# Performance work log

Hardware: AMD Instinct MI355X
Metric: run time of the kernel (lower is better)

Reference implementation:

```python
import jax, jax.numpy as jnp
import numpy as np

B, CQ, CR, HID, H, W = 8, 1024, 512, 256, 48, 48


def setup_inputs() -> dict:
    key = jax.random.key(0)
    ks = jax.random.split(key, 6)
    return {
        "query_features": jax.random.normal(ks[0], (B, CQ, H, W), dtype=jnp.float32),
        "reference_features": jax.random.normal(ks[1], (B, CR, H, W), dtype=jnp.float32),
        "Wq": jax.random.normal(ks[2], (HID, CQ), dtype=jnp.float32) * (1.0 / np.sqrt(CQ)),
        "bq": jax.random.normal(ks[3], (HID,), dtype=jnp.float32) * 0.01,
        "Wk": jax.random.normal(ks[4], (HID, CR), dtype=jnp.float32) * (1.0 / np.sqrt(CR)),
        "bk": jax.random.normal(ks[5], (HID,), dtype=jnp.float32) * 0.01,
    }


def reference(query_features, reference_features, Wq, bq, Wk, bk):
    b, _, h1, w1 = query_features.shape
    h2, w2 = reference_features.shape[-2:]
    # 1x1 convs == per-pixel linear projections
    Q = jnp.einsum("oc,bchw->bohw", Wq, query_features) + bq[None, :, None, None]
    K = jnp.einsum("oc,bchw->bohw", Wk, reference_features) + bk[None, :, None, None]
    # V: [b, c_ref, h2*w2]
    V = reference_features.reshape(b, reference_features.shape[1], h2 * w2)
    # attention logits: [b, h1, w1, h2*w2]
    attn = jnp.einsum("bcij,bckl->bijkl", Q, K).reshape(b, h1, w1, h2 * w2)
    attn = jax.nn.softmax(attn, axis=3)
    # weighted sum of V: [b, c_ref, h1, w1]
    attended = jnp.einsum("bijp,bcp->bcij", attn, V)
    return attended
```

## Files before the change

kernel.cpp:

```cpp
#include <hip/hip_runtime.h>

#define BB   8
#define PP   2304
#define CQD  1024
#define CRD  512
#define HIDD 256
#define GB   4
#define NKB  36
#define LOG2E 1.4426950408889634f

typedef float f32x4 __attribute__((ext_vector_type(4)));
typedef __bf16 bf16x8 __attribute__((ext_vector_type(8)));
typedef unsigned short u16x8 __attribute__((ext_vector_type(8)));
typedef unsigned short u16x4 __attribute__((ext_vector_type(4)));
typedef unsigned int u32x4 __attribute__((ext_vector_type(4)));
typedef unsigned short ushort_t;

__device__ __forceinline__ unsigned short f2bf(float f) {
  unsigned int u = __float_as_uint(f);
  u += 0x7fffu + ((u >> 16) & 1u);
  return (unsigned short)(u >> 16);
}
__device__ __forceinline__ float bf2f(unsigned short h) {
  return __uint_as_float(((unsigned int)h) << 16);
}
__device__ __forceinline__ bf16x8 load_bf8(const ushort_t* p) {
  return *(const bf16x8*)p;
}
__device__ __forceinline__ void async16(const void* g, void* l) {
  __builtin_amdgcn_global_load_lds(
      (const __attribute__((address_space(1))) unsigned int*)g,
      (__attribute__((address_space(3))) unsigned int*)l, 16, 0, 0);
}

#define MFMA16(a, b, c) __builtin_amdgcn_mfma_f32_16x16x32_bf16((a), (b), (c), 0, 0, 0)

__global__ __launch_bounds__(256) void wcast_kernel(
    const float* __restrict__ W, ushort_t* __restrict__ Wh,
    ushort_t* __restrict__ Wl) {
  const size_t i = ((size_t)blockIdx.x * 256 + threadIdx.x) * 8;
  float4 a = *(const float4*)(W + i);
  float4 b2 = *(const float4*)(W + i + 4);
  float av[8] = {a.x, a.y, a.z, a.w, b2.x, b2.y, b2.z, b2.w};
  u16x8 h, l;
#pragma unroll
  for (int j = 0; j < 8; ++j) {
    unsigned short hh = f2bf(av[j]);
    h[j] = hh;
    l[j] = f2bf(av[j] - bf2f(hh));
  }
  *(u16x8*)(Wh + i) = h;
  *(u16x8*)(Wl + i) = l;
}

template <int C, bool WV>
__global__ __launch_bounds__(256) void tcast_kernel(
    const float* __restrict__ X, ushort_t* __restrict__ Th,
    ushort_t* __restrict__ Tl, ushort_t* __restrict__ Vb) {
  const int b = blockIdx.z;
  const int p0 = blockIdx.x * 64;
  const int c0 = blockIdx.y * 64;
  const int tid = threadIdx.x;

  __shared__ unsigned int HL[64][66];

  {
    const int cr = tid >> 2;
    const int ch = tid & 3;
    const float* src = X + ((size_t)b * C + c0 + cr) * PP + p0 + ch * 16;
    u16x8 vcast[2];
#pragma unroll
    for (int i = 0; i < 4; ++i) {
      float4 v = *(const float4*)(src + i * 4);
      float vv[4] = {v.x, v.y, v.z, v.w};
#pragma unroll
      for (int k = 0; k < 4; ++k) {
        unsigned short h = f2bf(vv[k]);
        unsigned short l = f2bf(vv[k] - bf2f(h));
        HL[ch * 16 + i * 4 + k][cr] =
            (unsigned int)h | ((unsigned int)l << 16);
        if (WV) vcast[i >> 1][(i & 1) * 4 + k] = h;
      }
    }
    if (WV) {
      ushort_t* vd = Vb + ((size_t)b * C + c0 + cr) * PP + p0 + ch * 16;
      *(u16x8*)(vd) = vcast[0];
      *(u16x8*)(vd + 8) = vcast[1];
    }
  }
  __syncthreads();
  {
    const int pr = tid >> 2;
    const int pc = tid & 3;
    u16x8 hv[2], lv[2];
#pragma unroll
    for (int m = 0; m < 2; ++m)
#pragma unroll
      for (int j = 0; j < 8; ++j) {
        unsigned int wb = HL[pr][pc * 16 + m * 8 + j];
        hv[m][j] = (unsigned short)(wb & 0xffffu);
        lv[m][j] = (unsigned short)(wb >> 16);
      }
    const size_t obase = ((size_t)b * PP + p0 + pr) * C + c0 + pc * 16;
    *(u16x8*)(Th + obase) = hv[0];
    *(u16x8*)(Th + obase + 8) = hv[1];
    *(u16x8*)(Tl + obase) = lv[0];
    *(u16x8*)(Tl + obase + 8) = lv[1];
  }
}

template <int C>
__global__ __launch_bounds__(256, 2) void projgemm_kernel(
    const ushort_t* __restrict__ Wh, const ushort_t* __restrict__ Wl,
    const ushort_t* __restrict__ Xh, const ushort_t* __restrict__ Xl,
    const float* __restrict__ bias, ushort_t* __restrict__ Oh,
    ushort_t* __restrict__ Ol) {
  const int bp0 = blockIdx.x * 128;
  const int o0 = blockIdx.y * 128;
  const int tid = threadIdx.x;
  const int lane = tid & 63;
  const int w = tid >> 6;
  const int l15 = lane & 15;
  const int quad = lane >> 4;
  const int wm = w & 1;
  const int wn = w >> 1;

  __shared__ __align__(16) ushort_t AB[2][4][128][32];

  f32x4 acc[4][4] = {};

  const ushort_t* srcs[4] = {Wh + (size_t)o0 * C, Wl + (size_t)o0 * C,
                             Xh + (size_t)bp0 * C, Xl + (size_t)bp0 * C};
  const ushort_t* mysrc = srcs[w];
  const int r16 = lane >> 2;
  const int c8 = (lane & 3) * 8;

  auto stage = [&](int cs, int buf) {
    const ushort_t* sp = mysrc + cs * 32 + c8;
#pragma unroll
    for (int i = 0; i < 8; ++i)
      async16(sp + (size_t)(i * 16 + r16) * C, &AB[buf][w][i * 16][0]);
  };

  stage(0, 0);
  __syncthreads();

  const int NS = C / 32;
  for (int cs = 0; cs < NS; ++cs) {
    const int buf = cs & 1;
    if (cs + 1 < NS) stage(cs + 1, buf ^ 1);

    bf16x8 ah[4], al[4], bh[4], bl[4];
#pragma unroll
    for (int mt = 0; mt < 4; ++mt) {
      const int row = wm * 64 + mt * 16 + l15;
      ah[mt] = load_bf8(&AB[buf][0][row][quad * 8]);
      al[mt] = load_bf8(&AB[buf][1][row][quad * 8]);
    }
#pragma unroll
    for (int nt = 0; nt < 4; ++nt) {
      const int row = wn * 64 + nt * 16 + l15;
      bh[nt] = load_bf8(&AB[buf][2][row][quad * 8]);
      bl[nt] = load_bf8(&AB[buf][3][row][quad * 8]);
    }
#pragma unroll
    for (int mt = 0; mt < 4; ++mt)
#pragma unroll
      for (int nt = 0; nt < 4; ++nt) {
        acc[mt][nt] = MFMA16(ah[mt], bh[nt], acc[mt][nt]);
        acc[mt][nt] = MFMA16(al[mt], bh[nt], acc[mt][nt]);
        acc[mt][nt] = MFMA16(ah[mt], bl[nt], acc[mt][nt]);
      }
    __syncthreads();
  }

#pragma unroll
  for (int mt = 0; mt < 4; ++mt) {
    const int ob = o0 + wm * 64 + mt * 16 + quad * 4;
    float bv[4];
#pragma unroll
    for (int r = 0; r < 4; ++r) bv[r] = bias[ob + r];
#pragma unroll
    for (int nt = 0; nt < 4; ++nt) {
      const int bp = bp0 + wn * 64 + nt * 16 + l15;
      u16x4 hs, ls;
#pragma unroll
      for (int r = 0; r < 4; ++r) {
        float v2 = acc[mt][nt][r] + bv[r];
        unsigned short h = f2bf(v2);
        hs[r] = h;
        ls[r] = f2bf(v2 - bf2f(h));
      }
      const size_t base = (size_t)bp * HIDD + ob;
      *(u16x4*)(Oh + base) = hs;
      *(u16x4*)(Ol + base) = ls;
    }
  }
}

template <int C>
__global__ __launch_bounds__(256) void proj_kernel(
    const float* __restrict__ X, const float* __restrict__ W,
    const float* __restrict__ bias, ushort_t* __restrict__ Oh,
    ushort_t* __restrict__ Ol) {
  const int b = blockIdx.z;
  const int p0 = blockIdx.y * 64;
  const int o0 = blockIdx.x * 64;
  const int tid = threadIdx.x;
  const int lane = tid & 63;
  const int wave = tid >> 6;
  const int wm = wave & 1;
  const int wn = wave >> 1;
  const int l15 = lane & 15;
  const int quad = lane >> 4;

  __shared__ ushort_t Xh[64][40];
  __shared__ ushort_t Xl[64][40];

  f32x4 acc[2][2] = {};
  const float* Xb = X + (size_t)b * C * PP;
  const int cc = tid >> 3;
  const int ppo = (tid & 7) * 8;

  for (int c0 = 0; c0 < C; c0 += 32) {
    const float* src = Xb + (size_t)(c0 + cc) * PP + p0 + ppo;
    float4 v0 = *(const float4*)(src);
    float4 v1 = *(const float4*)(src + 4);
    float vv[8] = {v0.x, v0.y, v0.z, v0.w, v1.x, v1.y, v1.z, v1.w};
#pragma unroll
    for (int j = 0; j < 8; ++j) {
      unsigned short h = f2bf(vv[j]);
      Xh[ppo + j][cc] = h;
      Xl[ppo + j][cc] = f2bf(vv[j] - bf2f(h));
    }
    __syncthreads();

    bf16x8 wh[2], wl[2];
#pragma unroll
    for (int mt = 0; mt < 2; ++mt) {
      const float* wsrc =
          W + (size_t)(o0 + wm * 32 + mt * 16 + l15) * C + c0 + quad * 8;
      float4 a0 = *(const float4*)(wsrc);
      float4 a1 = *(const float4*)(wsrc + 4);
      float av[8] = {a0.x, a0.y, a0.z, a0.w, a1.x, a1.y, a1.z, a1.w};
      u16x8 hh, ll;
#pragma unroll
      for (int j = 0; j < 8; ++j) {
        unsigned short h = f2bf(av[j]);
        hh[j] = h;
        ll[j] = f2bf(av[j] - bf2f(h));
      }
      wh[mt] = __builtin_bit_cast(bf16x8, hh);
      wl[mt] = __builtin_bit_cast(bf16x8, ll);
    }

#pragma unroll
    for (int nt = 0; nt < 2; ++nt) {
      const int pr = wn * 32 + nt * 16 + l15;
      bf16x8 xh = load_bf8(&Xh[pr][quad * 8]);
      bf16x8 xl = load_bf8(&Xl[pr][quad * 8]);
#pragma unroll
      for (int mt = 0; mt < 2; ++mt) {
        acc[mt][nt] = MFMA16(wh[mt], xh, acc[mt][nt]);
        acc[mt][nt] = MFMA16(wl[mt], xh, acc[mt][nt]);
        acc[mt][nt] = MFMA16(wh[mt], xl, acc[mt][nt]);
      }
    }
    __syncthreads();
  }

#pragma unroll
  for (int mt = 0; mt < 2; ++mt) {
    const int ob = o0 + wm * 32 + mt * 16 + quad * 4;
#pragma unroll
    for (int nt = 0; nt < 2; ++nt) {
      const int p = p0 + wn * 32 + nt * 16 + l15;
      u16x4 hs, ls;
#pragma unroll
      for (int r = 0; r < 4; ++r) {
        float v = acc[mt][nt][r] + bias[ob + r];
        unsigned short h = f2bf(v);
        hs[r] = h;
        ls[r] = f2bf(v - bf2f(h));
      }
      const size_t base = ((size_t)b * PP + p) * HIDD + ob;
      *(u16x4*)(Oh + base) = hs;
      *(u16x4*)(Ol + base) = ls;
    }
  }
}

__global__ void cast_v_kernel(const float* __restrict__ X,
                              ushort_t* __restrict__ V) {
  const size_t i = ((size_t)blockIdx.x * 256 + threadIdx.x) * 4;
  float4 v = *(const float4*)(X + i);
  u16x4 o;
  o[0] = f2bf(v.x); o[1] = f2bf(v.y); o[2] = f2bf(v.z); o[3] = f2bf(v.w);
  *(u16x4*)(V + i) = o;
}

__global__ __launch_bounds__(256, 2) void sgemm_kernel(
    const ushort_t* __restrict__ Qh, const ushort_t* __restrict__ Ql,
    const ushort_t* __restrict__ Kh, const ushort_t* __restrict__ Kl,
    ushort_t* __restrict__ Pbuf, float* __restrict__ mpart,
    float* __restrict__ lpart, int bbase) {
  const int lin = blockIdx.x + 18 * blockIdx.y + 324 * blockIdx.z;
  const int o = (lin & 7) * 162 + (lin >> 3);
  const int b = o / 324;
  const int rem = o % 324;
  const int q0 = (rem % 18) * 128;
  const int k0 = (rem / 18) * 128;

  const int gb = bbase + b;
  const int tid = threadIdx.x;
  const int lane = tid & 63;
  const int w = tid >> 6;
  const int l15 = lane & 15;
  const int quad = lane >> 4;
  const int wm = w & 1;
  const int wn = w >> 1;

  __shared__ __align__(16) ushort_t AB[2][4][128][32];

  f32x4 acc[4][4] = {};

  const ushort_t* srcs[4] = {Qh + ((size_t)gb * PP + q0) * HIDD,
                             Ql + ((size_t)gb * PP + q0) * HIDD,
                             Kh + ((size_t)gb * PP + k0) * HIDD,
                             Kl + ((size_t)gb * PP + k0) * HIDD};
  const ushort_t* mysrc = srcs[w];
  const int r16 = lane >> 2;
  const int c8 = (lane & 3) * 8;

  auto stage = [&](int cs, int buf) {
    const ushort_t* sp = mysrc + cs * 32 + c8;
#pragma unroll
    for (int i = 0; i < 8; ++i)
      async16(sp + (size_t)(i * 16 + r16) * HIDD, &AB[buf][w][i * 16][0]);
  };

  stage(0, 0);
  __syncthreads();

  for (int cs = 0; cs < 8; ++cs) {
    const int buf = cs & 1;
    if (cs + 1 < 8) stage(cs + 1, buf ^ 1);

    bf16x8 ah[4], al[4], bh[4], bl[4];
#pragma unroll
    for (int mt = 0; mt < 4; ++mt) {
      const int row = wm * 64 + mt * 16 + l15;
      ah[mt] = load_bf8(&AB[buf][0][row][quad * 8]);
      al[mt] = load_bf8(&AB[buf][1][row][quad * 8]);
    }
#pragma unroll
    for (int nt = 0; nt < 4; ++nt) {
      const int row = wn * 64 + nt * 16 + l15;
      bh[nt] = load_bf8(&AB[buf][2][row][quad * 8]);
      bl[nt] = load_bf8(&AB[buf][3][row][quad * 8]);
    }
#pragma unroll
    for (int mt = 0; mt < 4; ++mt)
#pragma unroll
      for (int nt = 0; nt < 4; ++nt) {
        acc[mt][nt] = MFMA16(ah[mt], bh[nt], acc[mt][nt]);
        acc[mt][nt] = MFMA16(al[mt], bh[nt], acc[mt][nt]);
        acc[mt][nt] = MFMA16(ah[mt], bl[nt], acc[mt][nt]);
      }
    __syncthreads();
  }

  ushort_t* Pt = (ushort_t*)&AB[0][0][0][0];
  const int kb = (k0 >> 6) + wn;
#pragma unroll
  for (int mt = 0; mt < 4; ++mt) {
#pragma unroll
    for (int r = 0; r < 4; ++r) {
      float m = fmaxf(fmaxf(acc[mt][0][r], acc[mt][1][r]),
                      fmaxf(acc[mt][2][r], acc[mt][3][r]));
      m = fmaxf(m, __shfl_xor(m, 1));
      m = fmaxf(m, __shfl_xor(m, 2));
      m = fmaxf(m, __shfl_xor(m, 4));
      m = fmaxf(m, __shfl_xor(m, 8));
      float p0 = __expf(acc[mt][0][r] - m);
      float p1 = __expf(acc[mt][1][r] - m);
      float p2 = __expf(acc[mt][2][r] - m);
      float p3 = __expf(acc[mt][3][r] - m);
      float e = p0 + p1 + p2 + p3;
      e += __shfl_xor(e, 1);
      e += __shfl_xor(e, 2);
      e += __shfl_xor(e, 4);
      e += __shfl_xor(e, 8);
      const int row = wm * 64 + mt * 16 + quad * 4 + r;
      const int rx = row & 15;
      ushort_t* ptrow = Pt + row * 128;
      float pv[4] = {p0, p1, p2, p3};
#pragma unroll
      for (int nt = 0; nt < 4; ++nt) {
        const int col = wn * 64 + nt * 16 + l15;
        ptrow[(((col >> 3) ^ rx) << 3) + (col & 7)] = f2bf(pv[nt]);
      }
      if (l15 == 0) {
        const int q = q0 + row;
        mpart[((size_t)b * NKB + kb) * PP + q] = m;
        lpart[((size_t)b * NKB + kb) * PP + q] = e;
      }
    }
  }
  __syncthreads();
  {
    const int row = tid >> 1;
    const int half = tid & 1;
    const int rx = row & 15;
    const ushort_t* srcr = Pt + row * 128;
    ushort_t* dst = Pbuf + ((size_t)b * PP + q0 + row) * PP + k0 + half * 64;
#pragma unroll
    for (int j = 0; j < 8; ++j) {
      u16x8 v = *(const u16x8*)(srcr + (((half * 8 + j) ^ rx) << 3));
      *(u16x8*)(dst + j * 8) = v;
    }
  }
}

__global__ __launch_bounds__(256) void stats_kernel(
    const float* __restrict__ mpart, const float* __restrict__ lpart,
    float* __restrict__ alphab) {
  const int q = blockIdx.x * 256 + threadIdx.x;
  const int b = blockIdx.y;
  float m[NKB];
  float M = -3.0e38f;
#pragma unroll
  for (int kb = 0; kb < NKB; ++kb) {
    m[kb] = mpart[((size_t)b * NKB + kb) * PP + q];
    M = fmaxf(M, m[kb]);
  }
  float L = 0.f;
#pragma unroll
  for (int kb = 0; kb < NKB; ++kb)
    L += __expf(m[kb] - M) * lpart[((size_t)b * NKB + kb) * PP + q];
  const float rL = 1.f / L;
#pragma unroll
  for (int kb = 0; kb < NKB; ++kb)
    alphab[((size_t)b * NKB + kb) * PP + q] = __expf(m[kb] - M) * rL;
}

__global__ __launch_bounds__(256, 3) void pv_kernel(
    const ushort_t* __restrict__ Pb, const ushort_t* __restrict__ Vb,
    const float* __restrict__ alphab, float* __restrict__ out, int bbase) {
  const int lin = blockIdx.x + 36 * blockIdx.y + 144 * blockIdx.z;
  const int o = (lin & 7) * 72 + (lin >> 3);
  const int b = o / 144;
  const int m0 = (o % 36) * 64;
  const int n0 = ((o / 36) % 4) * 128;

  const int gb = bbase + b;
  const int tid = threadIdx.x;
  const int lane = tid & 63;
  const int w = tid >> 6;
  const int l15 = lane & 15;
  const int quad = lane >> 4;
  const int wm = w & 1;
  const int wn = w >> 1;

  __shared__ __align__(16) ushort_t Plds[2][64][64];
  __shared__ __align__(16) ushort_t Vt[2][128][64];

  f32x4 acc[2][4] = {};

  const ushort_t* P_base = Pb + ((size_t)b * PP + m0) * PP;
  const ushort_t* V_base = Vb + ((size_t)gb * CRD + n0) * PP;
  const float* a_base =
      alphab + (size_t)b * NKB * PP + m0 + wm * 32 + quad * 4;

  const int lr = lane >> 3;
  const int lc = lane & 7;

  auto stage = [&](int kb, int buf) {
#pragma unroll
    for (int j = 0; j < 2; ++j) {
      const int row = w * 16 + j * 8 + lr;
      const int ch = lc ^ (row & 7);
      async16(P_base + (size_t)row * PP + kb * 64 + ch * 8,
              &Plds[buf][w * 16 + j * 8][0]);
    }
#pragma unroll
    for (int j = 0; j < 4; ++j) {
      const int row = w * 32 + j * 8 + lr;
      const int ch = lc ^ (row & 7);
      async16(V_base + (size_t)row * PP + kb * 64 + ch * 8,
              &Vt[buf][w * 32 + j * 8][0]);
    }
  };

  stage(0, 0);
  __syncthreads();

  for (int kb = 0; kb < NKB; ++kb) {
    const int buf = kb & 1;
    if (kb + 1 < NKB) stage(kb + 1, buf ^ 1);

    f32x4 av[2];
#pragma unroll
    for (int mt = 0; mt < 2; ++mt)
      av[mt] = *(const f32x4*)(a_base + (size_t)kb * PP + mt * 16);

    f32x4 pacc[2][4] = {};
#pragma unroll
    for (int h = 0; h < 2; ++h) {
      bf16x8 pa[2], vf[4];
#pragma unroll
      for (int mt = 0; mt < 2; ++mt) {
        const int row = wm * 32 + mt * 16 + l15;
        const int g = (h * 4 + quad) ^ (row & 7);
        pa[mt] = load_bf8(&Plds[buf][row][g * 8]);
      }
#pragma unroll
      for (int nt = 0; nt < 4; ++nt) {
        const int row = wn * 64 + nt * 16 + l15;
        const int g = (h * 4 + quad) ^ (row & 7);
        vf[nt] = load_bf8(&Vt[buf][row][g * 8]);
      }
#pragma unroll
      for (int mt = 0; mt < 2; ++mt)
#pragma unroll
        for (int nt = 0; nt < 4; ++nt)
          pacc[mt][nt] = MFMA16(pa[mt], vf[nt], pacc[mt][nt]);
    }

#pragma unroll
    for (int mt = 0; mt < 2; ++mt)
#pragma unroll
      for (int nt = 0; nt < 4; ++nt)
        acc[mt][nt] += av[mt] * pacc[mt][nt];

    __syncthreads();
  }

#pragma unroll
  for (int mt = 0; mt < 2; ++mt) {
    const int q = m0 + wm * 32 + mt * 16 + quad * 4;
#pragma unroll
    for (int nt = 0; nt < 4; ++nt) {
      const int ch = n0 + wn * 64 + nt * 16 + l15;
      *(f32x4*)(out + ((size_t)gb * CRD + ch) * PP + q) = acc[mt][nt];
    }
  }
}

__global__ __launch_bounds__(256, 2) void attn_direct_kernel(
    const ushort_t* __restrict__ Qh, const ushort_t* __restrict__ Ql,
    const ushort_t* __restrict__ Kh, const ushort_t* __restrict__ Kl,
    const ushort_t* __restrict__ Vb, float* __restrict__ out) {
  const int b = blockIdx.z;
  const int qb = blockIdx.x;
  const int tid = threadIdx.x;
  const int lane = tid & 63;
  const int w = tid >> 6;
  const int l15 = lane & 15;
  const int quad = lane >> 4;

  __shared__ __align__(16) ushort_t Kbuf[2][2][16][520];
  __shared__ __align__(16) ushort_t P_lds[4][16][40];

  bf16x8 qh[8], ql[8];
  {
    const size_t qrow = ((size_t)b * PP + qb * 64 + w * 16 + l15) * HIDD;
#pragma unroll
    for (int ks = 0; ks < 8; ++ks) {
      qh[ks] = load_bf8(Qh + qrow + ks * 32 + quad * 8);
      ql[ks] = load_bf8(Ql + qrow + ks * 32 + quad * 8);
    }
  }

  f32x4 o_acc[32] = {};
  float m_run[4] = {-3.0e38f, -3.0e38f, -3.0e38f, -3.0e38f};
  float l_run[4] = {0.f, 0.f, 0.f, 0.f};

  const ushort_t* Kb[2] = {Kh + (size_t)b * PP * HIDD,
                           Kl + (size_t)b * PP * HIDD};
  const ushort_t* vbase = Vb + ((size_t)b * CRD + l15) * PP + quad * 8;

  auto stage = [&](int t, int buf) {
#pragma unroll
    for (int j = 0; j < 8; ++j) {
      const int idx = w * 8 + j;
      const int hl = idx >> 4;
      const int pair = idx & 15;
      const ushort_t* src =
          Kb[hl] + ((size_t)(t * 32 + pair * 2)) * HIDD + lane * 8;
      async16(src, &Kbuf[buf][hl][pair][0]);
    }
  };

  stage(0, 0);
  __syncthreads();

  for (int t = 0; t < PP / 32; ++t) {
    const int buf = t & 1;
    if (t + 1 < PP / 32) stage(t + 1, buf ^ 1);

    f32x4 sa0 = {}, sa1 = {};
#pragma unroll
    for (int ks = 0; ks < 8; ++ks) {
      const int co = (l15 & 1) * 256 + ks * 32 + quad * 8;
      bf16x8 kh0 = load_bf8(&Kbuf[buf][0][(l15 >> 1)][co]);
      bf16x8 kl0 = load_bf8(&Kbuf[buf][1][(l15 >> 1)][co]);
      bf16x8 kh1 = load_bf8(&Kbuf[buf][0][8 + (l15 >> 1)][co]);
      bf16x8 kl1 = load_bf8(&Kbuf[buf][1][8 + (l15 >> 1)][co]);
      sa0 = MFMA16(qh[ks], kh0, sa0);
      sa1 = MFMA16(qh[ks], kh1, sa1);
      sa0 = MFMA16(ql[ks], kh0, sa0);
      sa1 = MFMA16(ql[ks], kh1, sa1);
      sa0 = MFMA16(qh[ks], kl0, sa0);
      sa1 = MFMA16(qh[ks], kl1, sa1);
    }

    float mx[4], al[4], p0[4], p1[4], rs[4];
#pragma unroll
    for (int r = 0; r < 4; ++r) mx[r] = fmaxf(sa0[r], sa1[r]);
#pragma unroll
    for (int d = 1; d < 16; d <<= 1)
#pragma unroll
      for (int r = 0; r < 4; ++r) mx[r] = fmaxf(mx[r], __shfl_xor(mx[r], d));
#pragma unroll
    for (int r = 0; r < 4; ++r) {
      const float mnew = fmaxf(m_run[r], mx[r]);
      al[r] = __expf(m_run[r] - mnew);
      m_run[r] = mnew;
      p0[r] = __expf(sa0[r] - mnew);
      p1[r] = __expf(sa1[r] - mnew);
      rs[r] = p0[r] + p1[r];
    }
#pragma unroll
    for (int d = 1; d < 16; d <<= 1)
#pragma unroll
      for (int r = 0; r < 4; ++r) rs[r] += __shfl_xor(rs[r], d);
#pragma unroll
    for (int r = 0; r < 4; ++r) l_run[r] = l_run[r] * al[r] + rs[r];

#pragma unroll
    for (int r = 0; r < 4; ++r) {
      P_lds[w][quad * 4 + r][l15] = f2bf(p0[r]);
      P_lds[w][quad * 4 + r][16 + l15] = f2bf(p1[r]);
    }
    asm volatile("s_waitcnt lgkmcnt(0)" ::: "memory");
    bf16x8 pa = load_bf8(&P_lds[w][l15][quad * 8]);

#pragma unroll
    for (int nt = 0; nt < 32; ++nt)
#pragma unroll
      for (int r = 0; r < 4; ++r) o_acc[nt][r] *= al[r];

    const ushort_t* vt = vbase + t * 32;
#pragma unroll
    for (int nt = 0; nt < 32; ++nt) {
      bf16x8 vfr = load_bf8(vt + (size_t)nt * 16 * PP);
      o_acc[nt] = MFMA16(pa, vfr, o_acc[nt]);
    }
    __syncthreads();
  }

  float rl[4];
#pragma unroll
  for (int r = 0; r < 4; ++r) rl[r] = 1.f / l_run[r];
  const int q0 = qb * 64 + w * 16 + quad * 4;
#pragma unroll
  for (int nt = 0; nt < 32; ++nt) {
    const int c = nt * 16 + l15;
    float* op = out + ((size_t)b * CRD + c) * PP + q0;
#pragma unroll
    for (int r = 0; r < 4; ++r) op[r] = o_acc[nt][r] * rl[r];
  }
}

extern "C" void kernel_launch(void* const* d_in, const int* in_sizes, int n_in,
                              void* d_out, int out_size, void* d_ws,
                              size_t ws_size, hipStream_t stream) {
  (void)in_sizes; (void)n_in; (void)out_size;

  const float* Xq = (const float*)d_in[0];
  const float* Xr = (const float*)d_in[1];
  const float* Wq = (const float*)d_in[2];
  const float* bq = (const float*)d_in[3];
  const float* Wk = (const float*)d_in[4];
  const float* bk = (const float*)d_in[5];
  float* out = (float*)d_out;

  const size_t nQK = (size_t)BB * PP * HIDD;
  const size_t nV = (size_t)BB * CRD * PP;

  ushort_t* p = (ushort_t*)d_ws;
  ushort_t* Qh = p; p += nQK;
  ushort_t* Ql = p; p += nQK;
  ushort_t* Kh = p; p += nQK;
  ushort_t* Kl = p; p += nQK;
  ushort_t* Vb = p; p += nV;
  ushort_t* scratch = p;

  ushort_t* Pbuf = scratch;
  float* mpart = (float*)(Pbuf + (size_t)GB * PP * PP);
  float* lpart = mpart + (size_t)GB * NKB * PP;
  float* alphab = lpart + (size_t)GB * NKB * PP;
  char* attn_end = (char*)(alphab + (size_t)GB * NKB * PP);

  ushort_t* Xth = scratch;
  ushort_t* Xtl = Xth + (size_t)BB * PP * CQD;
  ushort_t* Wh2 = Xtl + (size_t)BB * PP * CQD;
  ushort_t* Wl2 = Wh2 + (size_t)HIDD * CQD;
  char* proj_end = (char*)(Wl2 + (size_t)HIDD * CQD);

  char* endp = proj_end > attn_end ? proj_end : attn_end;
  const size_t needed = (size_t)(endp - (char*)d_ws);

  if (ws_size >= needed) {
    wcast_kernel<<<dim3(HIDD * CQD / 2048), 256, 0, stream>>>(Wq, Wh2, Wl2);
    tcast_kernel<CQD, false><<<dim3(PP / 64, CQD / 64, BB), 256, 0, stream>>>(
        Xq, Xth, Xtl, nullptr);
    projgemm_kernel<CQD><<<dim3(BB * PP / 128, HIDD / 128), 256, 0, stream>>>(
        Wh2, Wl2, Xth, Xtl, bq, Qh, Ql);

    wcast_kernel<<<dim3(HIDD * CRD / 2048), 256, 0, stream>>>(Wk, Wh2, Wl2);
    tcast_kernel<CRD, true><<<dim3(PP / 64, CRD / 64, BB), 256, 0, stream>>>(
        Xr, Xth, Xtl, Vb);
    projgemm_kernel<CRD><<<dim3(BB * PP / 128, HIDD / 128), 256, 0, stream>>>(
        Wh2, Wl2, Xth, Xtl, bk, Kh, Kl);

    for (int g = 0; g < BB / GB; ++g) {
      const int bbase = g * GB;
      sgemm_kernel<<<dim3(PP / 128, PP / 128, GB), 256, 0, stream>>>(
          Qh, Ql, Kh, Kl, Pbuf, mpart, lpart, bbase);
      stats_kernel<<<dim3(PP / 256, GB), 256, 0, stream>>>(mpart, lpart,
                                                           alphab);
      pv_kernel<<<dim3(PP / 64, CRD / 128, GB), 256, 0, stream>>>(
          Pbuf, Vb, alphab, out, bbase);
    }
  } else {
    proj_kernel<CQD><<<dim3(4, PP / 64, BB), 256, 0, stream>>>(Xq, Wq, bq, Qh,
                                                               Ql);
    proj_kernel<CRD><<<dim3(4, PP / 64, BB), 256, 0, stream>>>(Xr, Wk, bk, Kh,
                                                               Kl);
    cast_v_kernel<<<dim3(nV / 1024), 256, 0, stream>>>(Xr, Vb);
    attn_direct_kernel<<<dim3(PP / 64, 1, BB), 256, 0, stream>>>(
        Qh, Ql, Kh, Kl, Vb, out);
  }
}
```

Measured before the change: 490.1 us.

## Split 3-term bf16 GEMM into sequential phases with half LDS and swizzle

The projection and score GEMMs used to stage hi and lo tiles of both operands together and issue three MFMAs per tile pair. They now run three sequential K-phases (hi*hi, lo*hi, hi*lo), each staging only one A and one B tile. This halves shared memory and the live fragment registers, which permits launch bounds of 4 blocks per CU, and it adds an XOR swizzle to cut LDS bank conflicts. The trade-off is three times as many loop iterations and barriers, and every operand tile is reloaded once per phase.

After: 570.3 us. +16.4%, slower.

```diff
diff --git a/kernel.cpp b/kernel.cpp
--- a/kernel.cpp
+++ b/kernel.cpp
@@ -110,7 +110,7 @@
 }
 
 template <int C>
-__global__ __launch_bounds__(256, 2) void projgemm_kernel(
+__global__ __launch_bounds__(256, 4) void projgemm_kernel(
     const ushort_t* __restrict__ Wh, const ushort_t* __restrict__ Wl,
     const ushort_t* __restrict__ Xh, const ushort_t* __restrict__ Xl,
     const float* __restrict__ bias, ushort_t* __restrict__ Oh,
@@ -125,52 +125,63 @@
   const int wm = w & 1;
   const int wn = w >> 1;
 
-  __shared__ __align__(16) ushort_t AB[2][4][128][32];
+  __shared__ __align__(16) ushort_t AB[2][2][128][32];
 
   f32x4 acc[4][4] = {};
 
-  const ushort_t* srcs[4] = {Wh + (size_t)o0 * C, Wl + (size_t)o0 * C,
-                             Xh + (size_t)bp0 * C, Xl + (size_t)bp0 * C};
-  const ushort_t* mysrc = srcs[w];
+  const ushort_t* Whb = Wh + (size_t)o0 * C;
+  const ushort_t* Wlb = Wl + (size_t)o0 * C;
+  const ushort_t* Xhb = Xh + (size_t)bp0 * C;
+  const ushort_t* Xlb = Xl + (size_t)bp0 * C;
+
+  const int sideB = w >> 1;
+  const int half = w & 1;
   const int r16 = lane >> 2;
-  const int c8 = (lane & 3) * 8;
+  const int c4 = lane & 3;
+  const int swz = c4 ^ ((r16 >> 1) & 3);
+
+  const int KS = C / 32;
+  const int NS = 3 * KS;
 
   auto stage = [&](int cs, int buf) {
-    const ushort_t* sp = mysrc + cs * 32 + c8;
-#pragma unroll
-    for (int i = 0; i < 8; ++i)
-      async16(sp + (size_t)(i * 16 + r16) * C, &AB[buf][w][i * 16][0]);
+    const int ph = cs / KS;
+    const int ko = (cs - ph * KS) * 32;
+    const ushort_t* base;
+    if (sideB)
+      base = (ph == 2) ? Xlb : Xhb;
+    else
+      base = (ph == 1) ? Wlb : Whb;
+    base += ko + swz * 8;
+#pragma unroll
+    for (int i = 0; i < 4; ++i) {
+      const int row = half * 64 + i * 16;
+      async16(base + (size_t)(row + r16) * C, &AB[buf][sideB][row][0]);
+    }
   };
 
   stage(0, 0);
   __syncthreads();
 
-  const int NS = C / 32;
   for (int cs = 0; cs < NS; ++cs) {
     const int buf = cs & 1;
     if (cs + 1 < NS) stage(cs + 1, buf ^ 1);
 
-    bf16x8 ah[4], al[4], bh[4], bl[4];
+    bf16x8 a[4], b[4];
 #pragma unroll
     for (int mt = 0; mt < 4; ++mt) {
       const int row = wm * 64 + mt * 16 + l15;
-      ah[mt] = load_bf8(&AB[buf][0][row][quad * 8]);
-      al[mt] = load_bf8(&AB[buf][1][row][quad * 8]);
+      a[mt] = load_bf8(&AB[buf][0][row][(quad ^ ((row >> 1) & 3)) * 8]);
     }
 #pragma unroll
     for (int nt = 0; nt < 4; ++nt) {
       const int row = wn * 64 + nt * 16 + l15;
-      bh[nt] = load_bf8(&AB[buf][2][row][quad * 8]);
-      bl[nt] = load_bf8(&AB[buf][3][row][quad * 8]);
+      b[nt] = load_bf8(&AB[buf][1][row][(quad ^ ((row >> 1) & 3)) * 8]);
     }
 #pragma unroll
     for (int mt = 0; mt < 4; ++mt)
 #pragma unroll
-      for (int nt = 0; nt < 4; ++nt) {
-        acc[mt][nt] = MFMA16(ah[mt], bh[nt], acc[mt][nt]);
-        acc[mt][nt] = MFMA16(al[mt], bh[nt], acc[mt][nt]);
-        acc[mt][nt] = MFMA16(ah[mt], bl[nt], acc[mt][nt]);
-      }
+      for (int nt = 0; nt < 4; ++nt)
+        acc[mt][nt] = MFMA16(a[mt], b[nt], acc[mt][nt]);
     __syncthreads();
   }
 
@@ -299,7 +310,7 @@
   *(u16x4*)(V + i) = o;
 }
 
-__global__ __launch_bounds__(256, 2) void sgemm_kernel(
+__global__ __launch_bounds__(256, 4) void sgemm_kernel(
     const ushort_t* __restrict__ Qh, const ushort_t* __restrict__ Ql,
     const ushort_t* __restrict__ Kh, const ushort_t* __restrict__ Kl,
     ushort_t* __restrict__ Pbuf, float* __restrict__ mpart,
@@ -320,53 +331,60 @@
   const int wm = w & 1;
   const int wn = w >> 1;
 
-  __shared__ __align__(16) ushort_t AB[2][4][128][32];
+  __shared__ __align__(16) ushort_t AB[2][2][128][32];
 
   f32x4 acc[4][4] = {};
 
-  const ushort_t* srcs[4] = {Qh + ((size_t)gb * PP + q0) * HIDD,
-                             Ql + ((size_t)gb * PP + q0) * HIDD,
-                             Kh + ((size_t)gb * PP + k0) * HIDD,
-                             Kl + ((size_t)gb * PP + k0) * HIDD};
-  const ushort_t* mysrc = srcs[w];
+  const ushort_t* Qhb = Qh + ((size_t)gb * PP + q0) * HIDD;
+  const ushort_t* Qlb = Ql + ((size_t)gb * PP + q0) * HIDD;
+  const ushort_t* Khb = Kh + ((size_t)gb * PP + k0) * HIDD;
+  const ushort_t* Klb = Kl + ((size_t)gb * PP + k0) * HIDD;
+
+  const int sideB = w >> 1;
+  const int half = w & 1;
   const int r16 = lane >> 2;
-  const int c8 = (lane & 3) * 8;
+  const int c4 = lane & 3;
+  const int swz = c4 ^ ((r16 >> 1) & 3);
 
   auto stage = [&](int cs, int buf) {
-    const ushort_t* sp = mysrc + cs * 32 + c8;
-#pragma unroll
-    for (int i = 0; i < 8; ++i)
-      async16(sp + (size_t)(i * 16 + r16) * HIDD, &AB[buf][w][i * 16][0]);
+    const int ph = cs >> 3;
+    const int ko = (cs & 7) * 32;
+    const ushort_t* base;
+    if (sideB)
+      base = (ph == 2) ? Klb : Khb;
+    else
+      base = (ph == 1) ? Qlb : Qhb;
+    base += ko + swz * 8;
+#pragma unroll
+    for (int i = 0; i < 4; ++i) {
+      const int row = half * 64 + i * 16;
+      async16(base + (size_t)(row + r16) * HIDD, &AB[buf][sideB][row][0]);
+    }
   };
 
   stage(0, 0);
   __syncthreads();
 
-  for (int cs = 0; cs < 8; ++cs) {
+  for (int cs = 0; cs < 24; ++cs) {
     const int buf = cs & 1;
-    if (cs + 1 < 8) stage(cs + 1, buf ^ 1);
-
-    bf16x8 ah[4], al[4], bh[4], bl[4];
+    if (cs + 1 < 24) stage(cs + 1, buf ^ 1);
+
+    bf16x8 a[4], b2[4];
 #pragma unroll
     for (int mt = 0; mt < 4; ++mt) {
       const int row = wm * 64 + mt * 16 + l15;
-      ah[mt] = load_bf8(&AB[buf][0][row][quad * 8]);
-      al[mt] = load_bf8(&AB[buf][1][row][quad * 8]);
+      a[mt] = load_bf8(&AB[buf][0][row][(quad ^ ((row >> 1) & 3)) * 8]);
     }
 #pragma unroll
     for (int nt = 0; nt < 4; ++nt) {
       const int row = wn * 64 + nt * 16 + l15;
-      bh[nt] = load_bf8(&AB[buf][2][row][quad * 8]);
-      bl[nt] = load_bf8(&AB[buf][3][row][quad * 8]);
+      b2[nt] = load_bf8(&AB[buf][1][row][(quad ^ ((row >> 1) & 3)) * 8]);
     }
 #pragma unroll
     for (int mt = 0; mt < 4; ++mt)
 #pragma unroll
-      for (int nt = 0; nt < 4; ++nt) {
-        acc[mt][nt] = MFMA16(ah[mt], bh[nt], acc[mt][nt]);
-        acc[mt][nt] = MFMA16(al[mt], bh[nt], acc[mt][nt]);
-        acc[mt][nt] = MFMA16(ah[mt], bl[nt], acc[mt][nt]);
-      }
+      for (int nt = 0; nt < 4; ++nt)
+        acc[mt][nt] = MFMA16(a[mt], b2[nt], acc[mt][nt]);
     __syncthreads();
   }
 
@@ -410,13 +428,13 @@
   __syncthreads();
   {
     const int row = tid >> 1;
-    const int half = tid & 1;
+    const int half2 = tid & 1;
     const int rx = row & 15;
     const ushort_t* srcr = Pt + row * 128;
-    ushort_t* dst = Pbuf + ((size_t)b * PP + q0 + row) * PP + k0 + half * 64;
+    ushort_t* dst = Pbuf + ((size_t)b * PP + q0 + row) * PP + k0 + half2 * 64;
 #pragma unroll
     for (int j = 0; j < 8; ++j) {
-      u16x8 v = *(const u16x8*)(srcr + (((half * 8 + j) ^ rx) << 3));
+      u16x8 v = *(const u16x8*)(srcr + (((half2 * 8 + j) ^ rx) << 3));
       *(u16x8*)(dst + j * 8) = v;
     }
   }
```
